# Kernel tuning notes

Hardware: AMD Instinct MI355X
Metric: run time of the kernel (lower is better)

The kernel has to match this reference:

```python
import jax, jax.numpy as jnp
import numpy as np

N, K, F, H, C = 16384, 16, 3, 64, 10


def setup_inputs() -> dict:
    key = jax.random.key(0)
    ks = jax.random.split(key, 6)
    pos = jax.random.normal(ks[0], (N, F), jnp.float32)
    batch = jnp.zeros((N,), jnp.int32)  # single graph
    W1 = jax.random.normal(ks[1], (2 * F, H), jnp.float32) * 0.1
    b1 = jnp.zeros((H,), jnp.float32)
    W2 = jax.random.normal(ks[2], (2 * H, H), jnp.float32) * 0.1
    b2 = jnp.zeros((H,), jnp.float32)
    Wc = jax.random.normal(ks[3], (H, C), jnp.float32) * 0.1
    bc = jnp.zeros((C,), jnp.float32)
    return {"pos": pos, "batch": batch, "W1": W1, "b1": b1,
            "W2": W2, "b2": b2, "Wc": Wc, "bc": bc}


def knn_graph(pos, k):
    # brute-force knn with self-loops (loop=True): self has distance 0
    sq = jnp.sum(pos * pos, axis=1)
    d = sq[:, None] + sq[None, :] - 2.0 * (pos @ pos.T)  # [N, N]
    _, idx = jax.lax.top_k(-d, k)  # [N, k] nearest neighbor indices (incl. self)
    return idx


def edge_conv(x, idx, W, b):
    # message for edge j->i: Linear(concat(x_i, x_j - x_i)); aggregate by max over neighbors
    n, k = idx.shape
    xi = x[:, None, :]               # [N, 1, F]
    xj = x[idx]                      # [N, k, F]
    msg = jnp.concatenate([jnp.broadcast_to(xi, (n, k, x.shape[1])), xj - xi], axis=-1)
    m = msg @ W + b                  # [N, k, H]
    return jnp.max(m, axis=1)        # [N, H]


def reference(pos, batch, W1, b1, W2, b2, Wc, bc):
    idx = knn_graph(pos, K)
    h = jax.nn.relu(edge_conv(pos, idx, W1, b1))
    h = jax.nn.relu(edge_conv(h, idx, W2, b2))
    g = jax.ops.segment_max(h, batch, num_segments=1)  # global max pool -> [1, H]
    return g @ Wc + bc
```

## Files before the change

### kernel.cpp

```cpp
#include <hip/hip_runtime.h>

#define NPTS 16384
#define KNN 16
#define HID 64
#define NCLS 10

#define WPB 4
#define QPB 8
#define SCAP 128
#define GRPQ 32
#define NGRP (NPTS / 128)
#define TQW 4
#define TPAD 576

typedef float v2f __attribute__((ext_vector_type(2)));

__device__ __forceinline__ v2f pdist(v2f Qx, v2f Qy, v2f Qz, v2f X, v2f Y, v2f Z, v2f W) {
    return __builtin_elementwise_fma(Qx, X,
            __builtin_elementwise_fma(Qy, Y,
             __builtin_elementwise_fma(Qz, Z, W)));
}

__device__ __forceinline__ float distm2(float qx, float qy, float qz, float4 c) {
    return fmaf(qx, c.x, fmaf(qy, c.y, fmaf(qz, c.z, c.w)));
}

__device__ __forceinline__ float __frfl(float x) {
    return __int_as_float(__builtin_amdgcn_readfirstlane(__float_as_int(x)));
}

__device__ __forceinline__ unsigned long long dkey(float v, int j) {
    unsigned u = __float_as_uint(v);
    u = (u & 0x80000000u) ? ~u : (u | 0x80000000u);
    return ((unsigned long long)u << 32) | (unsigned)j;
}

__device__ __forceinline__ unsigned long long shfl_xor_u64(unsigned long long x, int m) {
    unsigned hi = (unsigned)__shfl_xor((int)(x >> 32), m, 64);
    unsigned lo = (unsigned)__shfl_xor((int)(x & 0xffffffffu), m, 64);
    return ((unsigned long long)hi << 32) | lo;
}

__device__ __forceinline__ void wave_top16_16(unsigned long long (&key)[16], int lane,
                                              int q, int* __restrict__ idx) {
    int outj = 0x7fffffff;
    for (int r = 0; r < 16; ++r) {
        unsigned long long gm = key[0];
#pragma unroll
        for (int s = 1; s < 16; ++s) gm = key[s] < gm ? key[s] : gm;
#pragma unroll
        for (int st = 1; st < 64; st <<= 1) {
            unsigned long long o = shfl_xor_u64(gm, st);
            gm = o < gm ? o : gm;
        }
        if (lane == r) outj = (int)(gm & 0xffffffffu);
#pragma unroll
        for (int s = 0; s < 16; ++s)
            if (key[s] == gm) key[s] = ~0ull;
    }
    if (lane < 16) idx[q * KNN + lane] = outj;
}

__global__ void prep_kernel(const float* __restrict__ pos, float4* __restrict__ pos4,
                            float4* __restrict__ pm2, float4* __restrict__ pm2t) {
    int i = blockIdx.x * 256 + threadIdx.x;
    if (i < NPTS) {
        float x = pos[3 * i], y = pos[3 * i + 1], z = pos[3 * i + 2];
        float sq = fmaf(x, x, fmaf(y, y, z * z));
        pos4[i] = make_float4(x, y, z, sq);
        pm2[i] = make_float4(-2.f * x, -2.f * y, -2.f * z, sq);
    }
    if (i < NPTS / 2) {
        int p = i;
        float x0 = pos[6 * p],     y0 = pos[6 * p + 1], z0 = pos[6 * p + 2];
        float x1 = pos[6 * p + 3], y1 = pos[6 * p + 4], z1 = pos[6 * p + 5];
        float w0 = fmaf(x0, x0, fmaf(y0, y0, z0 * z0));
        float w1 = fmaf(x1, x1, fmaf(y1, y1, z1 * z1));
        int g = p >> 6, l = p & 63;
        pm2t[g * 128 + l]      = make_float4(-2.f * x0, -2.f * x1, -2.f * y0, -2.f * y1);
        pm2t[g * 128 + 64 + l] = make_float4(-2.f * z0, -2.f * z1, w0, w1);
    }
}

__global__ __launch_bounds__(256) void knn_tau_kernel(const float4* __restrict__ pos4,
                                                      const float4* __restrict__ pm2t,
                                                      float* __restrict__ tqg) {
    int lane = threadIdx.x & 63;
    int w = threadIdx.x >> 6;
    int q0 = (blockIdx.x * 4 + w) * TQW;
    v2f Qx[TQW], Qy[TQW], Qz[TQW];
#pragma unroll
    for (int i = 0; i < TQW; ++i) {
        float4 t4 = pos4[q0 + i];
        float ax = __frfl(t4.x), ay = __frfl(t4.y), az = __frfl(t4.z);
        Qx[i] = (v2f){ax, ax}; Qy[i] = (v2f){ay, ay}; Qz[i] = (v2f){az, az};
    }
    const float4* pt = pm2t + lane;
    int start = (((blockIdx.x >> 3) << 2) + w) & (NGRP - 1);
    float mn[TQW];
#pragma unroll
    for (int i = 0; i < TQW; ++i) mn[i] = INFINITY;
    {
        int g0 = start, g1 = (start + 1) & (NGRP - 1);
        int g2 = (start + 2) & (NGRP - 1), g3 = (start + 3) & (NGRP - 1);
        float4 aXY0 = pt[g0 * 128], aZW0 = pt[g0 * 128 + 64];
        float4 aXY1 = pt[g1 * 128], aZW1 = pt[g1 * 128 + 64];
        float4 bXY0 = pt[g2 * 128], bZW0 = pt[g2 * 128 + 64];
        float4 bXY1 = pt[g3 * 128], bZW1 = pt[g3 * 128 + 64];
#pragma unroll 2
        for (int t = 0; t < NGRP / 2; ++t) {
            v2f X0 = {aXY0.x, aXY0.y}, Y0 = {aXY0.z, aXY0.w};
            v2f Z0 = {aZW0.x, aZW0.y}, W0 = {aZW0.z, aZW0.w};
            v2f X1 = {aXY1.x, aXY1.y}, Y1 = {aXY1.z, aXY1.w};
            v2f Z1 = {aZW1.x, aZW1.y}, W1 = {aZW1.z, aZW1.w};
#pragma unroll
            for (int i = 0; i < TQW; ++i) {
                v2f D0 = pdist(Qx[i], Qy[i], Qz[i], X0, Y0, Z0, W0);
                v2f D1 = pdist(Qx[i], Qy[i], Qz[i], X1, Y1, Z1, W1);
                mn[i] = fminf(mn[i], fminf(D0.x, D0.y));
                mn[i] = fminf(mn[i], fminf(D1.x, D1.y));
            }
            int gp0 = (start + 2 * t + 4) & (NGRP - 1);
            int gp1 = (start + 2 * t + 5) & (NGRP - 1);
            aXY0 = bXY0; aZW0 = bZW0; aXY1 = bXY1; aZW1 = bZW1;
            bXY0 = pt[gp0 * 128]; bZW0 = pt[gp0 * 128 + 64];
            bXY1 = pt[gp1 * 128]; bZW1 = pt[gp1 * 128 + 64];
        }
    }
#pragma unroll
    for (int i = 0; i < TQW; ++i) {
        float m = mn[i];
        m = fminf(m, __shfl_xor(m, 16, 64));
        m = fminf(m, __shfl_xor(m, 32, 64));
        m = fmaxf(m, __shfl_xor(m, 1, 64));
        m = fmaxf(m, __shfl_xor(m, 2, 64));
        m = fmaxf(m, __shfl_xor(m, 4, 64));
        m = fmaxf(m, __shfl_xor(m, 8, 64));
        if (lane == 0) tqg[q0 + i] = m;
    }
}

__global__ __launch_bounds__(256) void knn_sel_kernel(const float4* __restrict__ pos4,
                                                      const float4* __restrict__ pm2,
                                                      const float4* __restrict__ pm2t,
                                                      const float* __restrict__ tqg,
                                                      int* __restrict__ idx) {
    __shared__ unsigned long long keys[QPB][SCAP];
    __shared__ int knt[QPB];
    int tid = threadIdx.x;
    int lane = tid & 63;
    int w = tid >> 6;
    int qb = blockIdx.x * QPB;
    v2f Qx[QPB], Qy[QPB], Qz[QPB];
    float tq[QPB];
#pragma unroll
    for (int i = 0; i < QPB; ++i) {
        float4 t4 = pos4[qb + i];
        float ax = __frfl(t4.x), ay = __frfl(t4.y), az = __frfl(t4.z);
        Qx[i] = (v2f){ax, ax}; Qy[i] = (v2f){ay, ay}; Qz[i] = (v2f){az, az};
        tq[i] = __frfl(tqg[qb + i]);
    }
    if (tid < QPB) knt[tid] = 0;
    __syncthreads();

    const float4* ptq = pm2t + (size_t)w * (GRPQ * 128) + lane;
    int pb0 = w * (GRPQ * 64);
    int start = (blockIdx.x >> 3) & (GRPQ - 1);
    {
        int g0 = start, g1 = (start + 1) & (GRPQ - 1);
        float4 aXY = ptq[g0 * 128], aZW = ptq[g0 * 128 + 64];
        float4 bXY = ptq[g1 * 128], bZW = ptq[g1 * 128 + 64];
#pragma unroll 1
        for (int t = 0; t < GRPQ; ++t) {
            v2f X = {aXY.x, aXY.y}, Y = {aXY.z, aXY.w};
            v2f Z = {aZW.x, aZW.y}, W = {aZW.z, aZW.w};
            int ga = (start + t) & (GRPQ - 1);
            int j0 = 2 * (pb0 + ga * 64 + lane);
#pragma unroll
            for (int i = 0; i < QPB; ++i) {
                v2f D = pdist(Qx[i], Qy[i], Qz[i], X, Y, Z, W);
                if (__any(fminf(D.x, D.y) <= tq[i])) {
                    if (D.x <= tq[i]) { int s = atomicAdd(&knt[i], 1); if (s < SCAP) keys[i][s] = dkey(D.x, j0); }
                    if (D.y <= tq[i]) { int s = atomicAdd(&knt[i], 1); if (s < SCAP) keys[i][s] = dkey(D.y, j0 + 1); }
                }
            }
            int gp = (start + t + 2) & (GRPQ - 1);
            aXY = bXY; aZW = bZW;
            bXY = ptq[gp * 128]; bZW = ptq[gp * 128 + 64];
        }
    }
    __syncthreads();

#pragma unroll
    for (int e = 0; e < 2; ++e) {
        int qi = w * 2 + e;
        int q = qb + qi;
        int ntot = knt[qi];
        if (ntot >= KNN && ntot <= SCAP) {
            unsigned long long k0 = (lane < ntot) ? keys[qi][lane] : ~0ull;
            unsigned long long k1 = (lane + 64 < ntot) ? keys[qi][lane + 64] : ~0ull;
            int r0 = 0, r1 = 0;
            int t = 0;
            for (; t + 8 <= ntot; t += 8) {
                unsigned long long a0 = keys[qi][t + 0], a1 = keys[qi][t + 1];
                unsigned long long a2 = keys[qi][t + 2], a3 = keys[qi][t + 3];
                unsigned long long a4 = keys[qi][t + 4], a5 = keys[qi][t + 5];
                unsigned long long a6 = keys[qi][t + 6], a7 = keys[qi][t + 7];
                r0 += (int)(a0 < k0) + (int)(a1 < k0) + (int)(a2 < k0) + (int)(a3 < k0)
                    + (int)(a4 < k0) + (int)(a5 < k0) + (int)(a6 < k0) + (int)(a7 < k0);
                r1 += (int)(a0 < k1) + (int)(a1 < k1) + (int)(a2 < k1) + (int)(a3 < k1)
                    + (int)(a4 < k1) + (int)(a5 < k1) + (int)(a6 < k1) + (int)(a7 < k1);
            }
            for (; t < ntot; ++t) {
                unsigned long long k = keys[qi][t];
                r0 += (int)(k < k0);
                r1 += (int)(k < k1);
            }
            if (lane < ntot && r0 < KNN) idx[q * KNN + r0] = (int)(k0 & 0xffffffffu);
            if (lane + 64 < ntot && r1 < KNN) idx[q * KNN + r1] = (int)(k1 & 0xffffffffu);
        } else {
            float tqq = (ntot > SCAP) ? tq[qi] : INFINITY;
            float ax = Qx[qi].x, ay = Qy[qi].x, az = Qz[qi].x;
            unsigned long long key[16];
#pragma unroll
            for (int u = 0; u < 16; ++u) key[u] = ~0ull;
            for (int j = lane; j < NPTS; j += 64) {
                float v = distm2(ax, ay, az, pm2[j]);
                unsigned long long k = dkey(v, j);
                if (v <= tqq && k < key[15]) {
#pragma unroll
                    for (int s = 0; s < 16; ++s) {
                        unsigned long long a = k < key[s] ? k : key[s];
                        unsigned long long b = k < key[s] ? key[s] : k;
                        key[s] = a;
                        k = b;
                    }
                }
            }
            wave_top16_16(key, lane, q, idx);
        }
    }
}

__global__ __launch_bounds__(256) void ec12_kernel(const float4* __restrict__ pos4,
                                                   const int* __restrict__ idx,
                                                   const float* __restrict__ W1,
                                                   const float* __restrict__ b1,
                                                   const float* __restrict__ W2,
                                                   const float* __restrict__ b2,
                                                   float* __restrict__ C2,
                                                   float* __restrict__ Y2) {
    __shared__ float h1s[16][64];
    int t = threadIdx.x & 63;
    int w = threadIdx.x >> 6;
    int pb = blockIdx.x * 16 + w * 4;
    float w0 = W1[0 * HID + t], w1 = W1[1 * HID + t], w2 = W1[2 * HID + t];
    float v0 = W1[3 * HID + t], v1 = W1[4 * HID + t], v2 = W1[5 * HID + t];
    float bt1 = b1[t];
#pragma unroll
    for (int i = 0; i < 4; ++i) {
        int p = pb + i;
        float4 xi = pos4[p];
        float C = bt1 + xi.x * (w0 - v0) + xi.y * (w1 - v1) + xi.z * (w2 - v2);
        const int4* ip = (const int4*)(idx + (size_t)p * KNN);
        int4 n0 = ip[0], n1 = ip[1], n2 = ip[2], n3 = ip[3];
        int jj[16] = {n0.x, n0.y, n0.z, n0.w, n1.x, n1.y, n1.z, n1.w,
                      n2.x, n2.y, n2.z, n2.w, n3.x, n3.y, n3.z, n3.w};
        float m = -INFINITY;
#pragma unroll
        for (int k = 0; k < KNN; ++k) {
            float4 xj = pos4[jj[k]];
            m = fmaxf(m, fmaf(xj.x, v0, fmaf(xj.y, v1, xj.z * v2)));
        }
        h1s[w * 4 + i][t] = fmaxf(C + m, 0.f);
    }
    __syncthreads();
    float aa[4] = {0.f, 0.f, 0.f, 0.f};
    float ab[4] = {0.f, 0.f, 0.f, 0.f};
#pragma unroll 8
    for (int f = 0; f < 64; ++f) {
        float wa = W2[f * HID + t];
        float wb = W2[(64 + f) * HID + t];
#pragma unroll
        for (int i = 0; i < 4; ++i) {
            float h = h1s[w * 4 + i][f];
            aa[i] = fmaf(h, wa, aa[i]);
            ab[i] = fmaf(h, wb, ab[i]);
        }
    }
    float bt = b2[t];
#pragma unroll
    for (int i = 0; i < 4; ++i) {
        C2[(pb + i) * HID + t] = bt + aa[i] - ab[i];
        Y2[(pb + i) * HID + t] = ab[i];
    }
}

__global__ __launch_bounds__(256) void ec2_maxpool_kernel(const float* __restrict__ C2,
                                                          const float* __restrict__ Y2,
                                                          const int* __restrict__ idx,
                                                          float* __restrict__ gpartial) {
    int t = threadIdx.x & 63;
    int lp = threadIdx.x >> 6;
    int p = blockIdx.x * 4 + lp;
    const int4* ip = (const int4*)(idx + (size_t)p * KNN);
    int4 n0 = ip[0], n1 = ip[1], n2 = ip[2], n3 = ip[3];
    int jj[16] = {n0.x, n0.y, n0.z, n0.w, n1.x, n1.y, n1.z, n1.w,
                  n2.x, n2.y, n2.z, n2.w, n3.x, n3.y, n3.z, n3.w};
    float m = -INFINITY;
#pragma unroll
    for (int k = 0; k < KNN; ++k) {
        m = fmaxf(m, Y2[jj[k] * HID + t]);
    }
    float val = fmaxf(C2[p * HID + t] + m, 0.f);
    __shared__ float red[4][64];
    red[lp][t] = val;
    __syncthreads();
    if (lp == 0) {
        float g = fmaxf(fmaxf(red[0][t], red[1][t]), fmaxf(red[2][t], red[3][t]));
        gpartial[blockIdx.x * 64 + t] = g;
    }
}

__global__ __launch_bounds__(256) void greduce2_kernel(const float* __restrict__ gpartial,
                                                       float* __restrict__ gp2) {
    __shared__ float red[4][64];
    int f = threadIdx.x & 63;
    int w = threadIdx.x >> 6;
    int r0 = blockIdx.x * 16 + w * 4;
    float m = -INFINITY;
#pragma unroll
    for (int r = 0; r < 4; ++r) m = fmaxf(m, gpartial[(r0 + r) * 64 + f]);
    red[w][f] = m;
    __syncthreads();
    if (w == 0)
        gp2[blockIdx.x * 64 + f] =
            fmaxf(fmaxf(red[0][f], red[1][f]), fmaxf(red[2][f], red[3][f]));
}

__global__ __launch_bounds__(256) void tail2_kernel(const float* __restrict__ gp2,
                                                    const float* __restrict__ Wc,
                                                    const float* __restrict__ bc,
                                                    float* __restrict__ out) {
    __shared__ float red[4][64];
    __shared__ float g[64];
    int f = threadIdx.x & 63;
    int w = threadIdx.x >> 6;
    float m = -INFINITY;
    for (int i = w; i < 256; i += 4) m = fmaxf(m, gp2[i * 64 + f]);
    red[w][f] = m;
    __syncthreads();
    if (w == 0) g[f] = fmaxf(fmaxf(red[0][f], red[1][f]), fmaxf(red[2][f], red[3][f]));
    __syncthreads();
    if (threadIdx.x < NCLS) {
        float a = bc[threadIdx.x];
#pragma unroll
        for (int h = 0; h < HID; ++h) a = fmaf(g[h], Wc[h * NCLS + threadIdx.x], a);
        out[threadIdx.x] = a;
    }
}

extern "C" void kernel_launch(void* const* d_in, const int* in_sizes, int n_in,
                              void* d_out, int out_size, void* d_ws, size_t ws_size,
                              hipStream_t stream) {
    const float* pos = (const float*)d_in[0];
    const float* W1 = (const float*)d_in[2];
    const float* b1 = (const float*)d_in[3];
    const float* W2 = (const float*)d_in[4];
    const float* b2 = (const float*)d_in[5];
    const float* Wc = (const float*)d_in[6];
    const float* bc = (const float*)d_in[7];
    float* out = (float*)d_out;

    char* ws = (char*)d_ws;
    size_t o = 0;
    auto alloc = [&](size_t bytes) { size_t r = o; o += (bytes + 255) & ~size_t(255); return r; };
    size_t fm = (size_t)NPTS * HID * 4;
    size_t o_pos4 = alloc((size_t)NPTS * 16);
    size_t o_pm2 = alloc((size_t)NPTS * 16);
    size_t o_pm2t = alloc((size_t)(NPTS + TPAD) * 16);
    size_t o_tqg = alloc((size_t)NPTS * 4);
    size_t o_idx = alloc((size_t)NPTS * KNN * 4);
    size_t o_C2 = alloc(fm);
    size_t o_Y2 = alloc(fm);
    size_t o_gp = alloc((size_t)(NPTS / 4) * HID * 4);
    size_t o_gp2 = alloc((size_t)256 * HID * 4);

    float4* pos4 = (float4*)(ws + o_pos4);
    float4* pm2 = (float4*)(ws + o_pm2);
    float4* pm2t = (float4*)(ws + o_pm2t);
    float* tqg = (float*)(ws + o_tqg);
    int* idx = (int*)(ws + o_idx);
    float* C2 = (float*)(ws + o_C2);
    float* Y2 = (float*)(ws + o_Y2);
    float* gp = (float*)(ws + o_gp);
    float* gp2 = (float*)(ws + o_gp2);

    prep_kernel<<<NPTS / 256, 256, 0, stream>>>(pos, pos4, pm2, pm2t);
    knn_tau_kernel<<<NPTS / (4 * TQW), 256, 0, stream>>>(pos4, pm2t, tqg);
    knn_sel_kernel<<<NPTS / QPB, 256, 0, stream>>>(pos4, pm2, pm2t, tqg, idx);
    ec12_kernel<<<NPTS / 16, 256, 0, stream>>>(pos4, idx, W1, b1, W2, b2, C2, Y2);
    ec2_maxpool_kernel<<<NPTS / 4, 256, 0, stream>>>(C2, Y2, idx, gp);
    greduce2_kernel<<<256, 256, 0, stream>>>(gp, gp2);
    tail2_kernel<<<1, 256, 0, stream>>>(gp2, Wc, bc, out);
}
```

Before: 309.0 us.

## Replace shared atomic candidate counters with per-wave ballot compaction segments

Candidate collection in the KNN select kernel now uses wave ballots and mbcnt to compute slot offsets in a per-wave segment of the key buffer, instead of atomicAdd on a shared counter per query. Per-wave counts are kept in registers and written once, and the key buffer is pre-filled with sentinel values so the rank pass can scan a fixed full length. This removes LDS atomic contention and serialisation in the hot loop. The per-wave cap of 32 can overflow more often than the shared cap of 128 and push queries to the slow brute-force fallback. The staggered group start order that spread memory access across blocks is also removed.

```diff
diff --git a/kernel.cpp b/kernel.cpp
--- a/kernel.cpp
+++ b/kernel.cpp
@@ -7,7 +7,8 @@
 
 #define WPB 4
 #define QPB 8
-#define SCAP 128
+#define SEG 32
+#define SCAP (WPB * SEG)
 #define GRPQ 32
 #define NGRP (NPTS / 128)
 #define TQW 4
@@ -27,6 +28,11 @@
 
 __device__ __forceinline__ float __frfl(float x) {
     return __int_as_float(__builtin_amdgcn_readfirstlane(__float_as_int(x)));
+}
+
+__device__ __forceinline__ int __mbcnt(unsigned long long m) {
+    return __builtin_amdgcn_mbcnt_hi((unsigned)(m >> 32),
+           __builtin_amdgcn_mbcnt_lo((unsigned)m, 0));
 }
 
 __device__ __forceinline__ unsigned long long dkey(float v, int j) {
@@ -146,7 +152,7 @@
                                                       const float* __restrict__ tqg,
                                                       int* __restrict__ idx) {
     __shared__ unsigned long long keys[QPB][SCAP];
-    __shared__ int knt[QPB];
+    __shared__ int cw[QPB][WPB];
     int tid = threadIdx.x;
     int lane = tid & 63;
     int w = tid >> 6;
@@ -160,34 +166,47 @@
         Qx[i] = (v2f){ax, ax}; Qy[i] = (v2f){ay, ay}; Qz[i] = (v2f){az, az};
         tq[i] = __frfl(tqg[qb + i]);
     }
-    if (tid < QPB) knt[tid] = 0;
+#pragma unroll
+    for (int u = 0; u < (QPB * SCAP) / 256; ++u)
+        ((unsigned long long*)keys)[u * 256 + tid] = ~0ull;
     __syncthreads();
 
     const float4* ptq = pm2t + (size_t)w * (GRPQ * 128) + lane;
     int pb0 = w * (GRPQ * 64);
-    int start = (blockIdx.x >> 3) & (GRPQ - 1);
+    int wq0 = 0, wq1 = 0, wq2 = 0, wq3 = 0, wq4 = 0, wq5 = 0, wq6 = 0, wq7 = 0;
     {
-        int g0 = start, g1 = (start + 1) & (GRPQ - 1);
-        float4 aXY = ptq[g0 * 128], aZW = ptq[g0 * 128 + 64];
-        float4 bXY = ptq[g1 * 128], bZW = ptq[g1 * 128 + 64];
+        float4 aXY = ptq[0], aZW = ptq[64];
+        float4 bXY = ptq[128], bZW = ptq[192];
 #pragma unroll 1
         for (int t = 0; t < GRPQ; ++t) {
             v2f X = {aXY.x, aXY.y}, Y = {aXY.z, aXY.w};
             v2f Z = {aZW.x, aZW.y}, W = {aZW.z, aZW.w};
-            int ga = (start + t) & (GRPQ - 1);
-            int j0 = 2 * (pb0 + ga * 64 + lane);
+            int j0 = 2 * (pb0 + t * 64 + lane);
 #pragma unroll
             for (int i = 0; i < QPB; ++i) {
                 v2f D = pdist(Qx[i], Qy[i], Qz[i], X, Y, Z, W);
-                if (__any(fminf(D.x, D.y) <= tq[i])) {
-                    if (D.x <= tq[i]) { int s = atomicAdd(&knt[i], 1); if (s < SCAP) keys[i][s] = dkey(D.x, j0); }
-                    if (D.y <= tq[i]) { int s = atomicAdd(&knt[i], 1); if (s < SCAP) keys[i][s] = dkey(D.y, j0 + 1); }
+                bool p0 = D.x <= tq[i], p1 = D.y <= tq[i];
+                unsigned long long m0 = __ballot(p0), m1 = __ballot(p1);
+                if (m0 | m1) {
+                    int wq = (i == 0) ? wq0 : (i == 1) ? wq1 : (i == 2) ? wq2 : (i == 3) ? wq3
+                           : (i == 4) ? wq4 : (i == 5) ? wq5 : (i == 6) ? wq6 : wq7;
+                    int c0 = __popcll(m0);
+                    if (p0) { int s = wq + __mbcnt(m0);      if (s < SEG) keys[i][w * SEG + s] = dkey(D.x, j0); }
+                    if (p1) { int s = wq + c0 + __mbcnt(m1); if (s < SEG) keys[i][w * SEG + s] = dkey(D.y, j0 + 1); }
+                    wq += c0 + __popcll(m1);
+                    if (i == 0) wq0 = wq; else if (i == 1) wq1 = wq; else if (i == 2) wq2 = wq;
+                    else if (i == 3) wq3 = wq; else if (i == 4) wq4 = wq; else if (i == 5) wq5 = wq;
+                    else if (i == 6) wq6 = wq; else wq7 = wq;
                 }
             }
-            int gp = (start + t + 2) & (GRPQ - 1);
             aXY = bXY; aZW = bZW;
-            bXY = ptq[gp * 128]; bZW = ptq[gp * 128 + 64];
-        }
+            bXY = ptq[(t + 2) * 128];
+            bZW = ptq[(t + 2) * 128 + 64];
+        }
+    }
+    if (lane == 0) {
+        cw[0][w] = wq0; cw[1][w] = wq1; cw[2][w] = wq2; cw[3][w] = wq3;
+        cw[4][w] = wq4; cw[5][w] = wq5; cw[6][w] = wq6; cw[7][w] = wq7;
     }
     __syncthreads();
 
@@ -195,13 +214,15 @@
     for (int e = 0; e < 2; ++e) {
         int qi = w * 2 + e;
         int q = qb + qi;
-        int ntot = knt[qi];
-        if (ntot >= KNN && ntot <= SCAP) {
-            unsigned long long k0 = (lane < ntot) ? keys[qi][lane] : ~0ull;
-            unsigned long long k1 = (lane + 64 < ntot) ? keys[qi][lane + 64] : ~0ull;
+        int c0 = cw[qi][0], c1 = cw[qi][1], c2 = cw[qi][2], c3 = cw[qi][3];
+        bool ovf = (c0 > SEG) | (c1 > SEG) | (c2 > SEG) | (c3 > SEG);
+        int ntot = min(c0, SEG) + min(c1, SEG) + min(c2, SEG) + min(c3, SEG);
+        if (!ovf && ntot >= KNN) {
+            unsigned long long k0 = keys[qi][lane];
+            unsigned long long k1 = keys[qi][lane + 64];
             int r0 = 0, r1 = 0;
-            int t = 0;
-            for (; t + 8 <= ntot; t += 8) {
+#pragma unroll 1
+            for (int t = 0; t < SCAP; t += 8) {
                 unsigned long long a0 = keys[qi][t + 0], a1 = keys[qi][t + 1];
                 unsigned long long a2 = keys[qi][t + 2], a3 = keys[qi][t + 3];
                 unsigned long long a4 = keys[qi][t + 4], a5 = keys[qi][t + 5];
@@ -211,15 +232,10 @@
                 r1 += (int)(a0 < k1) + (int)(a1 < k1) + (int)(a2 < k1) + (int)(a3 < k1)
                     + (int)(a4 < k1) + (int)(a5 < k1) + (int)(a6 < k1) + (int)(a7 < k1);
             }
-            for (; t < ntot; ++t) {
-                unsigned long long k = keys[qi][t];
-                r0 += (int)(k < k0);
-                r1 += (int)(k < k1);
-            }
-            if (lane < ntot && r0 < KNN) idx[q * KNN + r0] = (int)(k0 & 0xffffffffu);
-            if (lane + 64 < ntot && r1 < KNN) idx[q * KNN + r1] = (int)(k1 & 0xffffffffu);
+            if (r0 < KNN) idx[q * KNN + r0] = (int)(k0 & 0xffffffffu);
+            if (r1 < KNN) idx[q * KNN + r1] = (int)(k1 & 0xffffffffu);
         } else {
-            float tqq = (ntot > SCAP) ? tq[qi] : INFINITY;
+            float tqq = ovf ? tq[qi] : INFINITY;
             float ax = Qx[qi].x, ay = Qy[qi].x, az = Qz[qi].x;
             unsigned long long key[16];
 #pragma unroll
```

Measured after the change: 366.0 us. 18.4% more time.

## Assign queries per wave in kNN select, replace LDS atomics with ballot compaction

Applied to the files above, without the earlier changes.

The kNN selection kernel now gives each wave its own 4 queries and has it scan all candidate points, instead of 8 queries shared by 4 waves that each scan a quarter of the points. This removes the block-level barriers and shared counters. Candidate appends use ballot, popcount and mbcnt prefix offsets in place of per-lane LDS atomics. Two point groups are processed per iteration for more ILP, and the rank pass always scans the full 128 slots, pre-filled with max keys, with no tail loop. The trade-off is that each wave does more distance work per query batch, and the block count changes from NPTS/8 to NPTS/16.

```diff
diff --git a/kernel.cpp b/kernel.cpp
--- a/kernel.cpp
+++ b/kernel.cpp
@@ -6,9 +6,8 @@
 #define NCLS 10
 
 #define WPB 4
-#define QPB 8
+#define SQW 4
 #define SCAP 128
-#define GRPQ 32
 #define NGRP (NPTS / 128)
 #define TQW 4
 #define TPAD 576
@@ -27,6 +26,11 @@
 
 __device__ __forceinline__ float __frfl(float x) {
     return __int_as_float(__builtin_amdgcn_readfirstlane(__float_as_int(x)));
+}
+
+__device__ __forceinline__ int __mbcnt(unsigned long long m) {
+    return __builtin_amdgcn_mbcnt_hi((unsigned)(m >> 32),
+           __builtin_amdgcn_mbcnt_lo((unsigned)m, 0));
 }
 
 __device__ __forceinline__ unsigned long long dkey(float v, int j) {
@@ -145,82 +149,95 @@
                                                       const float4* __restrict__ pm2t,
                                                       const float* __restrict__ tqg,
                                                       int* __restrict__ idx) {
-    __shared__ unsigned long long keys[QPB][SCAP];
-    __shared__ int knt[QPB];
-    int tid = threadIdx.x;
-    int lane = tid & 63;
-    int w = tid >> 6;
-    int qb = blockIdx.x * QPB;
-    v2f Qx[QPB], Qy[QPB], Qz[QPB];
-    float tq[QPB];
-#pragma unroll
-    for (int i = 0; i < QPB; ++i) {
-        float4 t4 = pos4[qb + i];
+    __shared__ unsigned long long keys[WPB][SQW][SCAP];
+    int lane = threadIdx.x & 63;
+    int w = threadIdx.x >> 6;
+    int q0 = (blockIdx.x * 4 + w) * SQW;
+    v2f Qx[SQW], Qy[SQW], Qz[SQW];
+    float tq[SQW];
+#pragma unroll
+    for (int i = 0; i < SQW; ++i) {
+        float4 t4 = pos4[q0 + i];
         float ax = __frfl(t4.x), ay = __frfl(t4.y), az = __frfl(t4.z);
         Qx[i] = (v2f){ax, ax}; Qy[i] = (v2f){ay, ay}; Qz[i] = (v2f){az, az};
-        tq[i] = __frfl(tqg[qb + i]);
-    }
-    if (tid < QPB) knt[tid] = 0;
-    __syncthreads();
-
-    const float4* ptq = pm2t + (size_t)w * (GRPQ * 128) + lane;
-    int pb0 = w * (GRPQ * 64);
-    int start = (blockIdx.x >> 3) & (GRPQ - 1);
+        tq[i] = __frfl(tqg[q0 + i]);
+    }
+    unsigned long long* kb = &keys[w][0][0];
+#pragma unroll
+    for (int u = 0; u < (SQW * SCAP) / 64; ++u) kb[u * 64 + lane] = ~0ull;
+
+    const float4* pt = pm2t + lane;
+    int start = (((blockIdx.x >> 3) << 2) + w) & (NGRP - 1);
+    int wq[SQW] = {0, 0, 0, 0};
     {
-        int g0 = start, g1 = (start + 1) & (GRPQ - 1);
-        float4 aXY = ptq[g0 * 128], aZW = ptq[g0 * 128 + 64];
-        float4 bXY = ptq[g1 * 128], bZW = ptq[g1 * 128 + 64];
+        int g0 = start, g1 = (start + 1) & (NGRP - 1);
+        int g2 = (start + 2) & (NGRP - 1), g3 = (start + 3) & (NGRP - 1);
+        float4 aXY0 = pt[g0 * 128], aZW0 = pt[g0 * 128 + 64];
+        float4 aXY1 = pt[g1 * 128], aZW1 = pt[g1 * 128 + 64];
+        float4 bXY0 = pt[g2 * 128], bZW0 = pt[g2 * 128 + 64];
+        float4 bXY1 = pt[g3 * 128], bZW1 = pt[g3 * 128 + 64];
 #pragma unroll 1
-        for (int t = 0; t < GRPQ; ++t) {
-            v2f X = {aXY.x, aXY.y}, Y = {aXY.z, aXY.w};
-            v2f Z = {aZW.x, aZW.y}, W = {aZW.z, aZW.w};
-            int ga = (start + t) & (GRPQ - 1);
-            int j0 = 2 * (pb0 + ga * 64 + lane);
-#pragma unroll
-            for (int i = 0; i < QPB; ++i) {
-                v2f D = pdist(Qx[i], Qy[i], Qz[i], X, Y, Z, W);
-                if (__any(fminf(D.x, D.y) <= tq[i])) {
-                    if (D.x <= tq[i]) { int s = atomicAdd(&knt[i], 1); if (s < SCAP) keys[i][s] = dkey(D.x, j0); }
-                    if (D.y <= tq[i]) { int s = atomicAdd(&knt[i], 1); if (s < SCAP) keys[i][s] = dkey(D.y, j0 + 1); }
+        for (int t = 0; t < NGRP / 2; ++t) {
+            v2f X0 = {aXY0.x, aXY0.y}, Y0 = {aXY0.z, aXY0.w};
+            v2f Z0 = {aZW0.x, aZW0.y}, W0 = {aZW0.z, aZW0.w};
+            v2f X1 = {aXY1.x, aXY1.y}, Y1 = {aXY1.z, aXY1.w};
+            v2f Z1 = {aZW1.x, aZW1.y}, W1 = {aZW1.z, aZW1.w};
+            int ga = (start + 2 * t) & (NGRP - 1);
+            int gb = (start + 2 * t + 1) & (NGRP - 1);
+            int ja = 2 * (ga * 64 + lane);
+            int jb = 2 * (gb * 64 + lane);
+#pragma unroll
+            for (int i = 0; i < SQW; ++i) {
+                v2f D0 = pdist(Qx[i], Qy[i], Qz[i], X0, Y0, Z0, W0);
+                v2f D1 = pdist(Qx[i], Qy[i], Qz[i], X1, Y1, Z1, W1);
+                bool p0 = D0.x <= tq[i], p1 = D0.y <= tq[i];
+                bool p2 = D1.x <= tq[i], p3 = D1.y <= tq[i];
+                unsigned long long m0 = __ballot(p0), m1 = __ballot(p1);
+                unsigned long long m2 = __ballot(p2), m3 = __ballot(p3);
+                if (m0 | m1 | m2 | m3) {
+                    int c0 = __popcll(m0), c1 = __popcll(m1), c2 = __popcll(m2);
+                    int base = wq[i];
+                    unsigned long long* K = &keys[w][i][0];
+                    if (p0) { int s = base + __mbcnt(m0);                if (s < SCAP) K[s] = dkey(D0.x, ja); }
+                    if (p1) { int s = base + c0 + __mbcnt(m1);           if (s < SCAP) K[s] = dkey(D0.y, ja + 1); }
+                    if (p2) { int s = base + c0 + c1 + __mbcnt(m2);      if (s < SCAP) K[s] = dkey(D1.x, jb); }
+                    if (p3) { int s = base + c0 + c1 + c2 + __mbcnt(m3); if (s < SCAP) K[s] = dkey(D1.y, jb + 1); }
+                    wq[i] = base + c0 + c1 + c2 + __popcll(m3);
                 }
             }
-            int gp = (start + t + 2) & (GRPQ - 1);
-            aXY = bXY; aZW = bZW;
-            bXY = ptq[gp * 128]; bZW = ptq[gp * 128 + 64];
-        }
-    }
-    __syncthreads();
-
-#pragma unroll
-    for (int e = 0; e < 2; ++e) {
-        int qi = w * 2 + e;
-        int q = qb + qi;
-        int ntot = knt[qi];
-        if (ntot >= KNN && ntot <= SCAP) {
-            unsigned long long k0 = (lane < ntot) ? keys[qi][lane] : ~0ull;
-            unsigned long long k1 = (lane + 64 < ntot) ? keys[qi][lane + 64] : ~0ull;
+            int gp0 = (start + 2 * t + 4) & (NGRP - 1);
+            int gp1 = (start + 2 * t + 5) & (NGRP - 1);
+            aXY0 = bXY0; aZW0 = bZW0; aXY1 = bXY1; aZW1 = bZW1;
+            bXY0 = pt[gp0 * 128]; bZW0 = pt[gp0 * 128 + 64];
+            bXY1 = pt[gp1 * 128]; bZW1 = pt[gp1 * 128 + 64];
+        }
+    }
+
+#pragma unroll 1
+    for (int e = 0; e < SQW; ++e) {
+        int q = q0 + e;
+        int cnt = wq[e];
+        if (cnt >= KNN && cnt <= SCAP) {
+            const unsigned long long* K = &keys[w][e][0];
+            unsigned long long k0 = K[lane];
+            unsigned long long k1 = K[lane + 64];
             int r0 = 0, r1 = 0;
-            int t = 0;
-            for (; t + 8 <= ntot; t += 8) {
-                unsigned long long a0 = keys[qi][t + 0], a1 = keys[qi][t + 1];
-                unsigned long long a2 = keys[qi][t + 2], a3 = keys[qi][t + 3];
-                unsigned long long a4 = keys[qi][t + 4], a5 = keys[qi][t + 5];
-                unsigned long long a6 = keys[qi][t + 6], a7 = keys[qi][t + 7];
+#pragma unroll 1
+            for (int t = 0; t < SCAP; t += 8) {
+                unsigned long long a0 = K[t + 0], a1 = K[t + 1];
+                unsigned long long a2 = K[t + 2], a3 = K[t + 3];
+                unsigned long long a4 = K[t + 4], a5 = K[t + 5];
+                unsigned long long a6 = K[t + 6], a7 = K[t + 7];
                 r0 += (int)(a0 < k0) + (int)(a1 < k0) + (int)(a2 < k0) + (int)(a3 < k0)
                     + (int)(a4 < k0) + (int)(a5 < k0) + (int)(a6 < k0) + (int)(a7 < k0);
                 r1 += (int)(a0 < k1) + (int)(a1 < k1) + (int)(a2 < k1) + (int)(a3 < k1)
                     + (int)(a4 < k1) + (int)(a5 < k1) + (int)(a6 < k1) + (int)(a7 < k1);
             }
-            for (; t < ntot; ++t) {
-                unsigned long long k = keys[qi][t];
-                r0 += (int)(k < k0);
-                r1 += (int)(k < k1);
-            }
-            if (lane < ntot && r0 < KNN) idx[q * KNN + r0] = (int)(k0 & 0xffffffffu);
-            if (lane + 64 < ntot && r1 < KNN) idx[q * KNN + r1] = (int)(k1 & 0xffffffffu);
+            if (r0 < KNN) idx[q * KNN + r0] = (int)(k0 & 0xffffffffu);
+            if (r1 < KNN) idx[q * KNN + r1] = (int)(k1 & 0xffffffffu);
         } else {
-            float tqq = (ntot > SCAP) ? tq[qi] : INFINITY;
-            float ax = Qx[qi].x, ay = Qy[qi].x, az = Qz[qi].x;
+            float tqq = (cnt > SCAP) ? tq[e] : INFINITY;
+            float ax = Qx[e].x, ay = Qy[e].x, az = Qz[e].x;
             unsigned long long key[16];
 #pragma unroll
             for (int u = 0; u < 16; ++u) key[u] = ~0ull;
@@ -398,7 +415,7 @@
 
     prep_kernel<<<NPTS / 256, 256, 0, stream>>>(pos, pos4, pm2, pm2t);
     knn_tau_kernel<<<NPTS / (4 * TQW), 256, 0, stream>>>(pos4, pm2t, tqg);
-    knn_sel_kernel<<<NPTS / QPB, 256, 0, stream>>>(pos4, pm2, pm2t, tqg, idx);
+    knn_sel_kernel<<<NPTS / (4 * SQW), 256, 0, stream>>>(pos4, pm2, pm2t, tqg, idx);
     ec12_kernel<<<NPTS / 16, 256, 0, stream>>>(pos4, idx, W1, b1, W2, b2, C2, Y2);
     ec2_maxpool_kernel<<<NPTS / 4, 256, 0, stream>>>(C2, Y2, idx, gp);
     greduce2_kernel<<<256, 256, 0, stream>>>(gp, gp2);
```

New measurement: 321.3 us. +4.0%, slower.
